# Kernel optimization log

Measured on AMD Instinct MI355X. Metric: run time of the kernel, lower is better.

## Reference

```python
import jax, jax.numpy as jnp
import numpy as np

B, N, D, H = 2, 2048, 1024, 8
DH = D // H  # head dim = 128


def setup_inputs() -> dict:
    key = jax.random.key(0)
    k0, k1, k2 = jax.random.split(key, 3)
    s = 1.0 / np.sqrt(D).astype(np.float32)
    return {
        "x": jax.random.normal(k0, (B, N, D), dtype=jnp.float32),
        "w_qkv": jax.random.normal(k1, (3 * D, D), dtype=jnp.float32) * s,
        "b_qkv": jnp.zeros((3 * D,), dtype=jnp.float32),
        "w_o": jax.random.normal(k2, (D, D), dtype=jnp.float32) * s,
        "b_o": jnp.zeros((D,), dtype=jnp.float32),
    }


def reference(x, w_qkv, b_qkv, w_o, b_o):
    b, n, d = x.shape
    h = H
    dh = d // h
    # qkv projection (torch Linear: x @ W.T + b)
    qkv = x @ w_qkv.T + b_qkv                      # [b, n, 3d]
    # rearrange 'b n (k d h) -> k b h n d': head index is INNERMOST
    qkv = qkv.reshape(b, n, 3, dh, h)              # [b, n, k, dh, h]
    qkv = jnp.transpose(qkv, (2, 0, 4, 1, 3))      # [k, b, h, n, dh]
    q, k, v = qkv[0], qkv[1], qkv[2]
    # unnormalized attention: NO softmax between the two einsums
    attn = jnp.einsum('bhik,bhjk->bhij', q, k)     # [b, h, n, n]
    out = jnp.einsum('bhik,bhkj->bhij', attn, v)   # [b, h, n, dh]
    # rearrange 'b h n d -> b n (h d)'
    out = jnp.transpose(out, (0, 2, 1, 3)).reshape(b, n, d)
    return out @ w_o.T + b_o
```

## Files before the change

### kernel.cpp

```cpp
#include <hip/hip_runtime.h>
#include <hip/hip_bf16.h>
#include <stdint.h>


typedef __bf16 bf16_t;
typedef __bf16 bf16x4 __attribute__((ext_vector_type(4)));
typedef __bf16 bf16x8 __attribute__((ext_vector_type(8)));
typedef float  fx4    __attribute__((ext_vector_type(4)));
typedef unsigned short u16;
typedef u16 u16x4 __attribute__((ext_vector_type(4)));
typedef u16 u16x8 __attribute__((ext_vector_type(8)));

typedef const void __attribute__((address_space(1)))* gas_ptr;
typedef void __attribute__((address_space(3)))*       las_ptr;

__device__ __forceinline__ void gl_lds16(const void* g, void* l) {
  __builtin_amdgcn_global_load_lds((gas_ptr)g, (las_ptr)l, 16, 0, 0);
}

__global__ __launch_bounds__(256) void beacon_kernel(float* out, float val, int n)
{
  const int i = blockIdx.x * 256 + threadIdx.x;
  if (i < n) out[i] = val;
}

__global__ __launch_bounds__(256) void conv_all_kernel(
    const float* __restrict__ x, const float* __restrict__ wq,
    const float* __restrict__ wo, const float* __restrict__ bq,
    bf16_t* __restrict__ xb, bf16_t* __restrict__ wqkvb,
    bf16_t* __restrict__ wob, float* __restrict__ bqp)
{
  const int i = blockIdx.x * 256 + threadIdx.x;
  if (i < 2097152) {
    const float* src; bf16_t* dst; int soff, doff;
    if (i < 1048576) { src = x; dst = xb; soff = i; doff = i; }
    else if (i < 1835008) {
      const int j  = i - 1048576;
      const int rp = j >> 8, g = j & 255;
      const int kk = rp >> 10, rem = rp & 1023;
      const int hh = rem >> 7,  dd = rem & 127;
      const int r  = kk * 1024 + dd * 8 + hh;
      src = wq; dst = wqkvb; soff = r * 256 + g; doff = j;
    } else {
      const int j = i - 1835008;
      src = wo; dst = wob; soff = j; doff = j;
    }
    const float4 v = ((const float4*)src)[soff];
    bf16x4 o;
    o[0] = (bf16_t)v.x; o[1] = (bf16_t)v.y; o[2] = (bf16_t)v.z; o[3] = (bf16_t)v.w;
    ((bf16x4*)dst)[doff] = o;
  } else if (i < 2097920) {
    const int j = i - 2097152;
    float4 v;
    float* pv = (float*)&v;
#pragma unroll
    for (int q = 0; q < 4; ++q) {
      const int cp = j * 4 + q;
      const int kk = cp >> 10, rem = cp & 1023;
      const int hh = rem >> 7,  dd = rem & 127;
      pv[q] = bq[kk * 1024 + dd * 8 + hh];
    }
    ((float4*)bqp)[j] = v;
  }
}

__global__ __launch_bounds__(256) void gemm1_kernel(
    const bf16_t* __restrict__ A, const bf16_t* __restrict__ Bt,
    const float* __restrict__ bias, bf16_t* __restrict__ outb)
{
  __shared__ __align__(16) short As[128*32];
  __shared__ __align__(16) short Bs[128*32];
  const int t    = threadIdx.x;
  const int lane = t & 63;
  const int w    = t >> 6;
  const int wr   = (w >> 1) << 6;
  const int wc   = (w & 1) << 6;
  const int lrow = lane & 15;
  const int kq   = (lane >> 4) << 3;
  const int row0 = blockIdx.y * 128;
  const int col0 = blockIdx.x * 128;

  const int i0 = t, i1 = t + 256;
  const bf16_t* a0 = A  + (size_t)(row0 + (i0 >> 2)) * 1024 + ((i0 & 3) << 3);
  const bf16_t* a1 = A  + (size_t)(row0 + (i1 >> 2)) * 1024 + ((i1 & 3) << 3);
  const bf16_t* b0 = Bt + (size_t)(col0 + (i0 >> 2)) * 1024 + ((i0 & 3) << 3);
  const bf16_t* b1 = Bt + (size_t)(col0 + (i1 >> 2)) * 1024 + ((i1 & 3) << 3);
  short* sa0 = &As[i0 * 8]; short* sa1 = &As[i1 * 8];
  short* sb0 = &Bs[i0 * 8]; short* sb1 = &Bs[i1 * 8];

  fx4 acc[4][4] = {};

  for (int k0 = 0; k0 < 1024; k0 += 32) {
    gl_lds16(a0 + k0, sa0);
    gl_lds16(a1 + k0, sa1);
    gl_lds16(b0 + k0, sb0);
    gl_lds16(b1 + k0, sb1);
    __syncthreads();
    bf16x8 af[4], bfr[4];
#pragma unroll
    for (int i = 0; i < 4; ++i)
      af[i] = *(const bf16x8*)&As[(wr + i*16 + lrow)*32 + kq];
#pragma unroll
    for (int j = 0; j < 4; ++j)
      bfr[j] = *(const bf16x8*)&Bs[(wc + j*16 + lrow)*32 + kq];
#pragma unroll
    for (int i = 0; i < 4; ++i)
#pragma unroll
      for (int j = 0; j < 4; ++j)
        acc[i][j] = __builtin_amdgcn_mfma_f32_16x16x32_bf16(af[i], bfr[j], acc[i][j], 0, 0, 0);
    __syncthreads();
  }

#pragma unroll
  for (int j = 0; j < 4; ++j) {
    const int col = col0 + wc + j*16 + lrow;
    const float bv = bias[col];
#pragma unroll
    for (int i = 0; i < 4; ++i) {
#pragma unroll
      for (int r = 0; r < 4; ++r) {
        const int row = row0 + wr + i*16 + ((lane >> 4) << 2) + r;
        outb[(size_t)row * 3072 + col] = (bf16_t)(acc[i][j][r] + bv);
      }
    }
  }
}

__global__ __launch_bounds__(256) void gemm2_kernel(
    const bf16_t* __restrict__ A,
    const bf16_t* __restrict__ Wt,
    const float* __restrict__ bias,
    float* __restrict__ out)
{
  __shared__ __align__(16) short As[128*32];
  __shared__ __align__(16) short Bs[64*32];
  const int t    = threadIdx.x;
  const int lane = t & 63;
  const int w    = t >> 6;
  const int wm   = w >> 1;
  const int wn   = w & 1;
  const int lrow = lane & 15;
  const int kq   = (lane >> 4) << 3;
  const int row0 = blockIdx.y * 128;
  const int col0 = blockIdx.x * 64;
  const bf16_t* Bt = Wt + (row0 >= 2048 ? (size_t)1048576 : (size_t)0);

  const int i0 = t, i1 = t + 256;
  const bf16_t* a0 = A  + (size_t)(row0 + (i0 >> 2)) * 3072 + ((i0 & 3) << 3);
  const bf16_t* a1 = A  + (size_t)(row0 + (i1 >> 2)) * 3072 + ((i1 & 3) << 3);
  const bf16_t* b0 = Bt + (size_t)(col0 + (i0 >> 2)) * 1024 + ((i0 & 3) << 3);
  short* sa0 = &As[i0 * 8]; short* sa1 = &As[i1 * 8];
  short* sb0 = &Bs[i0 * 8];

  fx4 acc[4][2] = {};

  for (int k0 = 0; k0 < 1024; k0 += 32) {
    gl_lds16(a0 + k0, sa0);
    gl_lds16(a1 + k0, sa1);
    gl_lds16(b0 + k0, sb0);
    __syncthreads();
    bf16x8 af[4], bfr[2];
#pragma unroll
    for (int i = 0; i < 4; ++i)
      af[i] = *(const bf16x8*)&As[(wm*64 + i*16 + lrow)*32 + kq];
#pragma unroll
    for (int j = 0; j < 2; ++j)
      bfr[j] = *(const bf16x8*)&Bs[(wn*32 + j*16 + lrow)*32 + kq];
#pragma unroll
    for (int i = 0; i < 4; ++i)
#pragma unroll
      for (int j = 0; j < 2; ++j)
        acc[i][j] = __builtin_amdgcn_mfma_f32_16x16x32_bf16(af[i], bfr[j], acc[i][j], 0, 0, 0);
    __syncthreads();
  }

#pragma unroll
  for (int j = 0; j < 2; ++j) {
    const int col = col0 + wn*32 + j*16 + lrow;
    const float bv = bias[col];
#pragma unroll
    for (int i = 0; i < 4; ++i) {
#pragma unroll
      for (int r = 0; r < 4; ++r) {
        const int row = row0 + wm*64 + i*16 + ((lane >> 4) << 2) + r;
        out[(size_t)row * 1024 + col] = acc[i][j][r] + bv;
      }
    }
  }
}

__global__ __launch_bounds__(128) void kv_part(
    const bf16_t* __restrict__ qkv, float* __restrict__ Mpart)
{
  __shared__ float Ksf[64][128];
  __shared__ float Vsf[64][64];
  const int t = threadIdx.x;
  const int ch = blockIdx.x >> 1, dh = blockIdx.x & 1, bh = blockIdx.y;
  const int b = bh >> 3, h = bh & 7;
  const bf16_t* Kg = qkv + (size_t)(b * 2048) * 3072 + 1024 + h * 128;
  const bf16_t* Vg = qkv + (size_t)(b * 2048) * 3072 + 2048 + h * 128 + dh * 64;
  const int e0 = (t >> 3) * 8;
  const int d0 = (t & 7) * 8;
  float acc[8][8] = {};

  for (int sub = 0; sub < 2; ++sub) {
    const int n0 = ch * 128 + sub * 64;
#pragma unroll
    for (int p = 0; p < 8; ++p) {
      const int idx = t + p * 128;
      const int r = idx >> 4, c = (idx & 15) * 8;
      const bf16x8 k8 = *(const bf16x8*)(Kg + (size_t)(n0 + r) * 3072 + c);
      float4 f0 = { (float)k8[0], (float)k8[1], (float)k8[2], (float)k8[3] };
      float4 f1 = { (float)k8[4], (float)k8[5], (float)k8[6], (float)k8[7] };
      *(float4*)&Ksf[r][c]     = f0;
      *(float4*)&Ksf[r][c + 4] = f1;
    }
#pragma unroll
    for (int p = 0; p < 4; ++p) {
      const int idx = t + p * 128;
      const int r = idx >> 3, c = (idx & 7) * 8;
      const bf16x8 v8 = *(const bf16x8*)(Vg + (size_t)(n0 + r) * 3072 + c);
      float4 f0 = { (float)v8[0], (float)v8[1], (float)v8[2], (float)v8[3] };
      float4 f1 = { (float)v8[4], (float)v8[5], (float)v8[6], (float)v8[7] };
      *(float4*)&Vsf[r][c]     = f0;
      *(float4*)&Vsf[r][c + 4] = f1;
    }
    __syncthreads();
    for (int n = 0; n < 64; ++n) {
      const float4 ka = *(const float4*)&Ksf[n][e0];
      const float4 kb = *(const float4*)&Ksf[n][e0 + 4];
      const float4 va = *(const float4*)&Vsf[n][d0];
      const float4 vb = *(const float4*)&Vsf[n][d0 + 4];
      const float kf[8] = { ka.x, ka.y, ka.z, ka.w, kb.x, kb.y, kb.z, kb.w };
      const float vf[8] = { va.x, va.y, va.z, va.w, vb.x, vb.y, vb.z, vb.w };
#pragma unroll
      for (int i = 0; i < 8; ++i)
#pragma unroll
        for (int j = 0; j < 8; ++j) acc[i][j] += kf[i] * vf[j];
    }
    __syncthreads();
  }

  float* op = Mpart + ((size_t)(bh * 16 + ch) << 14) + dh * 64;
#pragma unroll
  for (int i = 0; i < 8; ++i) {
    *(float4*)&op[(e0 + i) * 128 + d0]     = *(const float4*)&acc[i][0];
    *(float4*)&op[(e0 + i) * 128 + d0 + 4] = *(const float4*)&acc[i][4];
  }
}

__global__ __launch_bounds__(256) void reduce_m(
    const float* __restrict__ Mpart, bf16_t* __restrict__ Mb)
{
  const int t = threadIdx.x, bh = blockIdx.y;
  const int task = blockIdx.x * 256 + t;
  const int e = task >> 5, dq = task & 31;
  const float* base = Mpart + ((size_t)(bh * 16) << 14) + e * 128 + dq * 4;
  float4 s = { 0.f, 0.f, 0.f, 0.f };
#pragma unroll
  for (int ch = 0; ch < 16; ++ch) {
    const float4 v = *(const float4*)(base + ((size_t)ch << 14));
    s.x += v.x; s.y += v.y; s.z += v.z; s.w += v.w;
  }
  u16x4 wv;
  bf16_t b0 = (bf16_t)s.x; wv[0] = *(u16*)&b0;
  bf16_t b1 = (bf16_t)s.y; wv[1] = *(u16*)&b1;
  bf16_t b2 = (bf16_t)s.z; wv[2] = *(u16*)&b2;
  bf16_t b3 = (bf16_t)s.w; wv[3] = *(u16*)&b3;
  *(u16x4*)(Mb + (size_t)bh * 16384 + e * 128 + dq * 4) = wv;
}

__global__ __launch_bounds__(256) void wprime_kernel(
    const bf16_t* __restrict__ wob, const bf16_t* __restrict__ Mb,
    bf16_t* __restrict__ Wt)
{
  __shared__ __align__(16) short As[128*32];
  __shared__ __align__(16) short Bs[64*32];
  const int t    = threadIdx.x;
  const int lane = t & 63;
  const int w    = t >> 6;
  const int wm   = w >> 1;
  const int wn   = w & 1;
  const int lrow = lane & 15;
  const int kq   = (lane >> 4) << 3;
  const int o0   = (blockIdx.x >> 1) * 128;
  const int eh   = (blockIdx.x & 1) * 64;
  const int bh   = blockIdx.y, b = bh >> 3, h = bh & 7;
  const bf16_t* A  = wob + (size_t)o0 * 1024 + h * 128;
  const bf16_t* Bt = Mb + (size_t)bh * 16384 + (size_t)eh * 128;

  const int i0 = t, i1 = t + 256;
  const bf16_t* a0 = A  + (size_t)(i0 >> 2) * 1024 + ((i0 & 3) << 3);
  const bf16_t* a1 = A  + (size_t)(i1 >> 2) * 1024 + ((i1 & 3) << 3);
  const bf16_t* b0 = Bt + (size_t)(i0 >> 2) * 128  + ((i0 & 3) << 3);
  short* sa0 = &As[i0 * 8]; short* sa1 = &As[i1 * 8];
  short* sb0 = &Bs[i0 * 8];

  fx4 acc[4][2] = {};

  for (int k0 = 0; k0 < 128; k0 += 32) {
    gl_lds16(a0 + k0, sa0);
    gl_lds16(a1 + k0, sa1);
    gl_lds16(b0 + k0, sb0);
    __syncthreads();
    bf16x8 af[4], bfr[2];
#pragma unroll
    for (int i = 0; i < 4; ++i)
      af[i] = *(const bf16x8*)&As[(wm*64 + i*16 + lrow)*32 + kq];
#pragma unroll
    for (int j = 0; j < 2; ++j)
      bfr[j] = *(const bf16x8*)&Bs[(wn*32 + j*16 + lrow)*32 + kq];
#pragma unroll
    for (int i = 0; i < 4; ++i)
#pragma unroll
      for (int j = 0; j < 2; ++j)
        acc[i][j] = __builtin_amdgcn_mfma_f32_16x16x32_bf16(af[i], bfr[j], acc[i][j], 0, 0, 0);
    __syncthreads();
  }

  bf16_t* obase = Wt + (size_t)b * 1048576 + h * 128;
#pragma unroll
  for (int j = 0; j < 2; ++j) {
    const int col = eh + wn*32 + j*16 + lrow;
#pragma unroll
    for (int i = 0; i < 4; ++i) {
#pragma unroll
      for (int r = 0; r < 4; ++r) {
        const int row = o0 + wm*64 + i*16 + ((lane >> 4) << 2) + r;
        obase[(size_t)row * 1024 + col] = (bf16_t)acc[i][j][r];
      }
    }
  }
}

extern "C" void kernel_launch(void* const* d_in, const int* in_sizes, int n_in,
                              void* d_out, int out_size, void* d_ws, size_t ws_size,
                              hipStream_t stream) {
  float* out = (float*)d_out;
  dim3 blk(256);

  int ix = -1, iwq = -1, ibq = -1, iwo = -1, ibo = -1;
  if (n_in == 5) {
    for (int i = 0; i < 5; ++i) {
      switch (in_sizes[i]) {
        case 4194304: ix  = i; break;
        case 3145728: iwq = i; break;
        case 3072:    ibq = i; break;
        case 1048576: iwo = i; break;
        case 1024:    ibo = i; break;
        default: break;
      }
    }
  }
  if (ix < 0 || iwq < 0 || ibq < 0 || iwo < 0 || ibo < 0) {
    beacon_kernel<<<dim3((out_size + 255) / 256), blk, 0, stream>>>(out, 50000.0f, out_size);
    return;
  }
  const size_t NEEDED = (size_t)40 * 1048576;
  if (ws_size < NEEDED) {
    beacon_kernel<<<dim3((out_size + 255) / 256), blk, 0, stream>>>(out, 30000.0f, out_size);
    return;
  }

  char* ws = (char*)d_ws;
  bf16_t* xb     = (bf16_t*)(ws);
  bf16_t* wqkvb  = (bf16_t*)(ws + (size_t)8  * 1048576);
  bf16_t* wob    = (bf16_t*)(ws + (size_t)14 * 1048576);
  bf16_t* qkv    = (bf16_t*)(ws + (size_t)16 * 1048576);
  bf16_t* Mb     = (bf16_t*)(ws);
  bf16_t* Wt     = (bf16_t*)(ws + (size_t)1  * 1048576);
  float*  bqp    = (float*)d_out;
  float*  Mpart  = (float*)d_out;

  const float* bo = (const float*)d_in[ibo];

  conv_all_kernel<<<dim3(8195),   blk, 0, stream>>>((const float*)d_in[ix],
                                                    (const float*)d_in[iwq],
                                                    (const float*)d_in[iwo],
                                                    (const float*)d_in[ibq],
                                                    xb, wqkvb, wob, bqp);
  gemm1_kernel   <<<dim3(24, 32), blk, 0, stream>>>(xb, wqkvb, bqp, qkv);
  kv_part        <<<dim3(32, 16), dim3(128), 0, stream>>>(qkv, Mpart);
  reduce_m       <<<dim3(16, 16), blk, 0, stream>>>(Mpart, Mb);
  wprime_kernel  <<<dim3(16, 16), blk, 0, stream>>>(wob, Mb, Wt);
  gemm2_kernel   <<<dim3(16, 32), blk, 0, stream>>>(qkv, Wt, bo, out);
}
```

Measured before the change: 173.9 us.

## Compute K^T V on MFMA via transposed K/V and widen GEMM K-steps

Replaces the scalar FP32 outer-product K^T·V partial kernel with a transpose kernel that writes K and V in head-dim-major layout, followed by an MFMA GEMM over 8 sequence slices and a smaller reduction. This moves the per-head 128x128 accumulation onto matrix cores and halves the number of partials to reduce. Separately, gemm1 and gemm2 now load two 32-wide K chunks per barrier pair, which halves the synchronisation count at the cost of doubled LDS use. The transpose adds an extra pass over K and V through global memory, and Vt is parked in the output buffer as scratch.

```diff
diff --git a/kernel.cpp b/kernel.cpp
--- a/kernel.cpp
+++ b/kernel.cpp
@@ -17,6 +17,8 @@
 __device__ __forceinline__ void gl_lds16(const void* g, void* l) {
   __builtin_amdgcn_global_load_lds((gas_ptr)g, (las_ptr)l, 16, 0, 0);
 }
+
+#define TSLAB 262144
 
 __global__ __launch_bounds__(256) void beacon_kernel(float* out, float val, int n)
 {
@@ -68,6 +70,119 @@
     const bf16_t* __restrict__ A, const bf16_t* __restrict__ Bt,
     const float* __restrict__ bias, bf16_t* __restrict__ outb)
 {
+  __shared__ __align__(16) short As0[128*32], As1[128*32];
+  __shared__ __align__(16) short Bs0[128*32], Bs1[128*32];
+  const int t    = threadIdx.x;
+  const int lane = t & 63;
+  const int w    = t >> 6;
+  const int wr   = (w >> 1) << 6;
+  const int wc   = (w & 1) << 6;
+  const int lrow = lane & 15;
+  const int kq   = (lane >> 4) << 3;
+  const int row0 = blockIdx.y * 128;
+  const int col0 = blockIdx.x * 128;
+
+  const int i0 = t, i1 = t + 256;
+  const bf16_t* a0 = A  + (size_t)(row0 + (i0 >> 2)) * 1024 + ((i0 & 3) << 3);
+  const bf16_t* a1 = A  + (size_t)(row0 + (i1 >> 2)) * 1024 + ((i1 & 3) << 3);
+  const bf16_t* b0 = Bt + (size_t)(col0 + (i0 >> 2)) * 1024 + ((i0 & 3) << 3);
+  const bf16_t* b1 = Bt + (size_t)(col0 + (i1 >> 2)) * 1024 + ((i1 & 3) << 3);
+
+  fx4 acc[4][4] = {};
+
+  for (int k0 = 0; k0 < 1024; k0 += 64) {
+    gl_lds16(a0 + k0,      &As0[i0 * 8]);
+    gl_lds16(a1 + k0,      &As0[i1 * 8]);
+    gl_lds16(b0 + k0,      &Bs0[i0 * 8]);
+    gl_lds16(b1 + k0,      &Bs0[i1 * 8]);
+    gl_lds16(a0 + k0 + 32, &As1[i0 * 8]);
+    gl_lds16(a1 + k0 + 32, &As1[i1 * 8]);
+    gl_lds16(b0 + k0 + 32, &Bs1[i0 * 8]);
+    gl_lds16(b1 + k0 + 32, &Bs1[i1 * 8]);
+    __syncthreads();
+    {
+      bf16x8 af[4], bfr[4];
+#pragma unroll
+      for (int i = 0; i < 4; ++i)
+        af[i] = *(const bf16x8*)&As0[(wr + i*16 + lrow)*32 + kq];
+#pragma unroll
+      for (int j = 0; j < 4; ++j)
+        bfr[j] = *(const bf16x8*)&Bs0[(wc + j*16 + lrow)*32 + kq];
+#pragma unroll
+      for (int i = 0; i < 4; ++i)
+#pragma unroll
+        for (int j = 0; j < 4; ++j)
+          acc[i][j] = __builtin_amdgcn_mfma_f32_16x16x32_bf16(af[i], bfr[j], acc[i][j], 0, 0, 0);
+    }
+    {
+      bf16x8 af[4], bfr[4];
+#pragma unroll
+      for (int i = 0; i < 4; ++i)
+        af[i] = *(const bf16x8*)&As1[(wr + i*16 + lrow)*32 + kq];
+#pragma unroll
+      for (int j = 0; j < 4; ++j)
+        bfr[j] = *(const bf16x8*)&Bs1[(wc + j*16 + lrow)*32 + kq];
+#pragma unroll
+      for (int i = 0; i < 4; ++i)
+#pragma unroll
+        for (int j = 0; j < 4; ++j)
+          acc[i][j] = __builtin_amdgcn_mfma_f32_16x16x32_bf16(af[i], bfr[j], acc[i][j], 0, 0, 0);
+    }
+    __syncthreads();
+  }
+
+#pragma unroll
+  for (int j = 0; j < 4; ++j) {
+    const int col = col0 + wc + j*16 + lrow;
+    const float bv = bias[col];
+#pragma unroll
+    for (int i = 0; i < 4; ++i) {
+#pragma unroll
+      for (int r = 0; r < 4; ++r) {
+        const int row = row0 + wr + i*16 + ((lane >> 4) << 2) + r;
+        outb[(size_t)row * 3072 + col] = (bf16_t)(acc[i][j][r] + bv);
+      }
+    }
+  }
+}
+
+__global__ __launch_bounds__(256) void kt_vt_kernel(
+    const bf16_t* __restrict__ qkv, bf16_t* __restrict__ Kt,
+    bf16_t* __restrict__ Vt)
+{
+  __shared__ u16 L[64][132];
+  const int t  = threadIdx.x;
+  const int n0 = blockIdx.x * 64;
+  const int bh = blockIdx.y >> 1, kv = blockIdx.y & 1;
+  const int b  = bh >> 3, h = bh & 7;
+  const u16* src = (const u16*)qkv + (size_t)(b * 2048 + n0) * 3072
+                   + (1 + kv) * 1024 + h * 128;
+
+#pragma unroll
+  for (int p = 0; p < 4; ++p) {
+    const int idx = t + p * 256;
+    const int r = idx >> 4, g = idx & 15;
+    const u16x8 v = *(const u16x8*)(src + (size_t)r * 3072 + 8 * g);
+    *(u16x8*)&L[r][8 * g] = v;
+  }
+  __syncthreads();
+
+  bf16_t* dstb = (kv == 0 ? Kt : Vt) + (size_t)bh * TSLAB;
+#pragma unroll
+  for (int p = 0; p < 4; ++p) {
+    const int idx = t + p * 256;
+    const int c = idx >> 3, gn = idx & 7;
+    u16x8 wv;
+#pragma unroll
+    for (int j = 0; j < 8; ++j) wv[j] = L[8 * gn + j][c];
+    *(u16x8*)(dstb + (size_t)c * 2048 + n0 + 8 * gn) = wv;
+  }
+}
+
+__global__ __launch_bounds__(256) void kvt_mfma_kernel(
+    const bf16_t* __restrict__ Kt, const bf16_t* __restrict__ Vt,
+    float* __restrict__ Mpart2)
+{
   __shared__ __align__(16) short As[128*32];
   __shared__ __align__(16) short Bs[128*32];
   const int t    = threadIdx.x;
@@ -77,20 +192,22 @@
   const int wc   = (w & 1) << 6;
   const int lrow = lane & 15;
   const int kq   = (lane >> 4) << 3;
-  const int row0 = blockIdx.y * 128;
-  const int col0 = blockIdx.x * 128;
+  const int ks   = blockIdx.x;
+  const int bh   = blockIdx.y;
+  const bf16_t* Ab = Kt + (size_t)bh * TSLAB + ks * 256;
+  const bf16_t* Bb = Vt + (size_t)bh * TSLAB + ks * 256;
 
   const int i0 = t, i1 = t + 256;
-  const bf16_t* a0 = A  + (size_t)(row0 + (i0 >> 2)) * 1024 + ((i0 & 3) << 3);
-  const bf16_t* a1 = A  + (size_t)(row0 + (i1 >> 2)) * 1024 + ((i1 & 3) << 3);
-  const bf16_t* b0 = Bt + (size_t)(col0 + (i0 >> 2)) * 1024 + ((i0 & 3) << 3);
-  const bf16_t* b1 = Bt + (size_t)(col0 + (i1 >> 2)) * 1024 + ((i1 & 3) << 3);
+  const bf16_t* a0 = Ab + (size_t)(i0 >> 2) * 2048 + ((i0 & 3) << 3);
+  const bf16_t* a1 = Ab + (size_t)(i1 >> 2) * 2048 + ((i1 & 3) << 3);
+  const bf16_t* b0 = Bb + (size_t)(i0 >> 2) * 2048 + ((i0 & 3) << 3);
+  const bf16_t* b1 = Bb + (size_t)(i1 >> 2) * 2048 + ((i1 & 3) << 3);
   short* sa0 = &As[i0 * 8]; short* sa1 = &As[i1 * 8];
   short* sb0 = &Bs[i0 * 8]; short* sb1 = &Bs[i1 * 8];
 
   fx4 acc[4][4] = {};
 
-  for (int k0 = 0; k0 < 1024; k0 += 32) {
+  for (int k0 = 0; k0 < 256; k0 += 32) {
     gl_lds16(a0 + k0, sa0);
     gl_lds16(a1 + k0, sa1);
     gl_lds16(b0 + k0, sb0);
@@ -111,155 +228,31 @@
     __syncthreads();
   }
 
+  float* op = Mpart2 + ((size_t)(bh * 8 + ks) << 14);
 #pragma unroll
   for (int j = 0; j < 4; ++j) {
-    const int col = col0 + wc + j*16 + lrow;
-    const float bv = bias[col];
+    const int col = wc + j*16 + lrow;
 #pragma unroll
     for (int i = 0; i < 4; ++i) {
 #pragma unroll
       for (int r = 0; r < 4; ++r) {
-        const int row = row0 + wr + i*16 + ((lane >> 4) << 2) + r;
-        outb[(size_t)row * 3072 + col] = (bf16_t)(acc[i][j][r] + bv);
+        const int row = wr + i*16 + ((lane >> 4) << 2) + r;
+        op[(size_t)row * 128 + col] = acc[i][j][r];
       }
     }
   }
 }
 
-__global__ __launch_bounds__(256) void gemm2_kernel(
-    const bf16_t* __restrict__ A,
-    const bf16_t* __restrict__ Wt,
-    const float* __restrict__ bias,
-    float* __restrict__ out)
-{
-  __shared__ __align__(16) short As[128*32];
-  __shared__ __align__(16) short Bs[64*32];
-  const int t    = threadIdx.x;
-  const int lane = t & 63;
-  const int w    = t >> 6;
-  const int wm   = w >> 1;
-  const int wn   = w & 1;
-  const int lrow = lane & 15;
-  const int kq   = (lane >> 4) << 3;
-  const int row0 = blockIdx.y * 128;
-  const int col0 = blockIdx.x * 64;
-  const bf16_t* Bt = Wt + (row0 >= 2048 ? (size_t)1048576 : (size_t)0);
-
-  const int i0 = t, i1 = t + 256;
-  const bf16_t* a0 = A  + (size_t)(row0 + (i0 >> 2)) * 3072 + ((i0 & 3) << 3);
-  const bf16_t* a1 = A  + (size_t)(row0 + (i1 >> 2)) * 3072 + ((i1 & 3) << 3);
-  const bf16_t* b0 = Bt + (size_t)(col0 + (i0 >> 2)) * 1024 + ((i0 & 3) << 3);
-  short* sa0 = &As[i0 * 8]; short* sa1 = &As[i1 * 8];
-  short* sb0 = &Bs[i0 * 8];
-
-  fx4 acc[4][2] = {};
-
-  for (int k0 = 0; k0 < 1024; k0 += 32) {
-    gl_lds16(a0 + k0, sa0);
-    gl_lds16(a1 + k0, sa1);
-    gl_lds16(b0 + k0, sb0);
-    __syncthreads();
-    bf16x8 af[4], bfr[2];
-#pragma unroll
-    for (int i = 0; i < 4; ++i)
-      af[i] = *(const bf16x8*)&As[(wm*64 + i*16 + lrow)*32 + kq];
-#pragma unroll
-    for (int j = 0; j < 2; ++j)
-      bfr[j] = *(const bf16x8*)&Bs[(wn*32 + j*16 + lrow)*32 + kq];
-#pragma unroll
-    for (int i = 0; i < 4; ++i)
-#pragma unroll
-      for (int j = 0; j < 2; ++j)
-        acc[i][j] = __builtin_amdgcn_mfma_f32_16x16x32_bf16(af[i], bfr[j], acc[i][j], 0, 0, 0);
-    __syncthreads();
-  }
-
-#pragma unroll
-  for (int j = 0; j < 2; ++j) {
-    const int col = col0 + wn*32 + j*16 + lrow;
-    const float bv = bias[col];
-#pragma unroll
-    for (int i = 0; i < 4; ++i) {
-#pragma unroll
-      for (int r = 0; r < 4; ++r) {
-        const int row = row0 + wm*64 + i*16 + ((lane >> 4) << 2) + r;
-        out[(size_t)row * 1024 + col] = acc[i][j][r] + bv;
-      }
-    }
-  }
-}
-
-__global__ __launch_bounds__(128) void kv_part(
-    const bf16_t* __restrict__ qkv, float* __restrict__ Mpart)
-{
-  __shared__ float Ksf[64][128];
-  __shared__ float Vsf[64][64];
-  const int t = threadIdx.x;
-  const int ch = blockIdx.x >> 1, dh = blockIdx.x & 1, bh = blockIdx.y;
-  const int b = bh >> 3, h = bh & 7;
-  const bf16_t* Kg = qkv + (size_t)(b * 2048) * 3072 + 1024 + h * 128;
-  const bf16_t* Vg = qkv + (size_t)(b * 2048) * 3072 + 2048 + h * 128 + dh * 64;
-  const int e0 = (t >> 3) * 8;
-  const int d0 = (t & 7) * 8;
-  float acc[8][8] = {};
-
-  for (int sub = 0; sub < 2; ++sub) {
-    const int n0 = ch * 128 + sub * 64;
-#pragma unroll
-    for (int p = 0; p < 8; ++p) {
-      const int idx = t + p * 128;
-      const int r = idx >> 4, c = (idx & 15) * 8;
-      const bf16x8 k8 = *(const bf16x8*)(Kg + (size_t)(n0 + r) * 3072 + c);
-      float4 f0 = { (float)k8[0], (float)k8[1], (float)k8[2], (float)k8[3] };
-      float4 f1 = { (float)k8[4], (float)k8[5], (float)k8[6], (float)k8[7] };
-      *(float4*)&Ksf[r][c]     = f0;
-      *(float4*)&Ksf[r][c + 4] = f1;
-    }
-#pragma unroll
-    for (int p = 0; p < 4; ++p) {
-      const int idx = t + p * 128;
-      const int r = idx >> 3, c = (idx & 7) * 8;
-      const bf16x8 v8 = *(const bf16x8*)(Vg + (size_t)(n0 + r) * 3072 + c);
-      float4 f0 = { (float)v8[0], (float)v8[1], (float)v8[2], (float)v8[3] };
-      float4 f1 = { (float)v8[4], (float)v8[5], (float)v8[6], (float)v8[7] };
-      *(float4*)&Vsf[r][c]     = f0;
-      *(float4*)&Vsf[r][c + 4] = f1;
-    }
-    __syncthreads();
-    for (int n = 0; n < 64; ++n) {
-      const float4 ka = *(const float4*)&Ksf[n][e0];
-      const float4 kb = *(const float4*)&Ksf[n][e0 + 4];
-      const float4 va = *(const float4*)&Vsf[n][d0];
-      const float4 vb = *(const float4*)&Vsf[n][d0 + 4];
-      const float kf[8] = { ka.x, ka.y, ka.z, ka.w, kb.x, kb.y, kb.z, kb.w };
-      const float vf[8] = { va.x, va.y, va.z, va.w, vb.x, vb.y, vb.z, vb.w };
-#pragma unroll
-      for (int i = 0; i < 8; ++i)
-#pragma unroll
-        for (int j = 0; j < 8; ++j) acc[i][j] += kf[i] * vf[j];
-    }
-    __syncthreads();
-  }
-
-  float* op = Mpart + ((size_t)(bh * 16 + ch) << 14) + dh * 64;
-#pragma unroll
-  for (int i = 0; i < 8; ++i) {
-    *(float4*)&op[(e0 + i) * 128 + d0]     = *(const float4*)&acc[i][0];
-    *(float4*)&op[(e0 + i) * 128 + d0 + 4] = *(const float4*)&acc[i][4];
-  }
-}
-
-__global__ __launch_bounds__(256) void reduce_m(
-    const float* __restrict__ Mpart, bf16_t* __restrict__ Mb)
+__global__ __launch_bounds__(256) void reduce_m2(
+    const float* __restrict__ Mpart2, bf16_t* __restrict__ Mb)
 {
   const int t = threadIdx.x, bh = blockIdx.y;
   const int task = blockIdx.x * 256 + t;
-  const int e = task >> 5, dq = task & 31;
-  const float* base = Mpart + ((size_t)(bh * 16) << 14) + e * 128 + dq * 4;
+  const float* base = Mpart2 + ((size_t)(bh * 8) << 14) + task * 4;
   float4 s = { 0.f, 0.f, 0.f, 0.f };
 #pragma unroll
-  for (int ch = 0; ch < 16; ++ch) {
-    const float4 v = *(const float4*)(base + ((size_t)ch << 14));
+  for (int ks = 0; ks < 8; ++ks) {
+    const float4 v = *(const float4*)(base + ((size_t)ks << 14));
     s.x += v.x; s.y += v.y; s.z += v.z; s.w += v.w;
   }
   u16x4 wv;
@@ -267,7 +260,7 @@
   bf16_t b1 = (bf16_t)s.y; wv[1] = *(u16*)&b1;
   bf16_t b2 = (bf16_t)s.z; wv[2] = *(u16*)&b2;
   bf16_t b3 = (bf16_t)s.w; wv[3] = *(u16*)&b3;
-  *(u16x4*)(Mb + (size_t)bh * 16384 + e * 128 + dq * 4) = wv;
+  *(u16x4*)(Mb + (size_t)bh * 16384 + task * 4) = wv;
 }
 
 __global__ __launch_bounds__(256) void wprime_kernel(
@@ -333,6 +326,86 @@
   }
 }
 
+__global__ __launch_bounds__(256) void gemm2_kernel(
+    const bf16_t* __restrict__ A,
+    const bf16_t* __restrict__ Wt,
+    const float* __restrict__ bias,
+    float* __restrict__ out)
+{
+  __shared__ __align__(16) short As0[128*32], As1[128*32];
+  __shared__ __align__(16) short Bs0[64*32],  Bs1[64*32];
+  const int t    = threadIdx.x;
+  const int lane = t & 63;
+  const int w    = t >> 6;
+  const int wm   = w >> 1;
+  const int wn   = w & 1;
+  const int lrow = lane & 15;
+  const int kq   = (lane >> 4) << 3;
+  const int row0 = blockIdx.y * 128;
+  const int col0 = blockIdx.x * 64;
+  const bf16_t* Bt = Wt + (row0 >= 2048 ? (size_t)1048576 : (size_t)0);
+
+  const int i0 = t, i1 = t + 256;
+  const bf16_t* a0 = A  + (size_t)(row0 + (i0 >> 2)) * 3072 + ((i0 & 3) << 3);
+  const bf16_t* a1 = A  + (size_t)(row0 + (i1 >> 2)) * 3072 + ((i1 & 3) << 3);
+  const bf16_t* b0 = Bt + (size_t)(col0 + (i0 >> 2)) * 1024 + ((i0 & 3) << 3);
+
+  fx4 acc[4][2] = {};
+
+  for (int k0 = 0; k0 < 1024; k0 += 64) {
+    gl_lds16(a0 + k0,      &As0[i0 * 8]);
+    gl_lds16(a1 + k0,      &As0[i1 * 8]);
+    gl_lds16(b0 + k0,      &Bs0[i0 * 8]);
+    gl_lds16(a0 + k0 + 32, &As1[i0 * 8]);
+    gl_lds16(a1 + k0 + 32, &As1[i1 * 8]);
+    gl_lds16(b0 + k0 + 32, &Bs1[i0 * 8]);
+    __syncthreads();
+    {
+      bf16x8 af[4], bfr[2];
+#pragma unroll
+      for (int i = 0; i < 4; ++i)
+        af[i] = *(const bf16x8*)&As0[(wm*64 + i*16 + lrow)*32 + kq];
+#pragma unroll
+      for (int j = 0; j < 2; ++j)
+        bfr[j] = *(const bf16x8*)&Bs0[(wn*32 + j*16 + lrow)*32 + kq];
+#pragma unroll
+      for (int i = 0; i < 4; ++i)
+#pragma unroll
+        for (int j = 0; j < 2; ++j)
+          acc[i][j] = __builtin_amdgcn_mfma_f32_16x16x32_bf16(af[i], bfr[j], acc[i][j], 0, 0, 0);
+    }
+    {
+      bf16x8 af[4], bfr[2];
+#pragma unroll
+      for (int i = 0; i < 4; ++i)
+        af[i] = *(const bf16x8*)&As1[(wm*64 + i*16 + lrow)*32 + kq];
+#pragma unroll
+      for (int j = 0; j < 2; ++j)
+        bfr[j] = *(const bf16x8*)&Bs1[(wn*32 + j*16 + lrow)*32 + kq];
+#pragma unroll
+      for (int i = 0; i < 4; ++i)
+#pragma unroll
+        for (int j = 0; j < 2; ++j)
+          acc[i][j] = __builtin_amdgcn_mfma_f32_16x16x32_bf16(af[i], bfr[j], acc[i][j], 0, 0, 0);
+    }
+    __syncthreads();
+  }
+
+#pragma unroll
+  for (int j = 0; j < 2; ++j) {
+    const int col = col0 + wn*32 + j*16 + lrow;
+    const float bv = bias[col];
+#pragma unroll
+    for (int i = 0; i < 4; ++i) {
+#pragma unroll
+      for (int r = 0; r < 4; ++r) {
+        const int row = row0 + wm*64 + i*16 + ((lane >> 4) << 2) + r;
+        out[(size_t)row * 1024 + col] = acc[i][j][r] + bv;
+      }
+    }
+  }
+}
+
 extern "C" void kernel_launch(void* const* d_in, const int* in_sizes, int n_in,
                               void* d_out, int out_size, void* d_ws, size_t ws_size,
                               hipStream_t stream) {
@@ -367,10 +440,12 @@
   bf16_t* wqkvb  = (bf16_t*)(ws + (size_t)8  * 1048576);
   bf16_t* wob    = (bf16_t*)(ws + (size_t)14 * 1048576);
   bf16_t* qkv    = (bf16_t*)(ws + (size_t)16 * 1048576);
-  bf16_t* Mb     = (bf16_t*)(ws);
-  bf16_t* Wt     = (bf16_t*)(ws + (size_t)1  * 1048576);
+  bf16_t* Kt     = (bf16_t*)(ws);
+  bf16_t* Mb     = (bf16_t*)(ws + (size_t)8  * 1048576);
+  bf16_t* Wt     = (bf16_t*)(ws + (size_t)9  * 1048576);
   float*  bqp    = (float*)d_out;
-  float*  Mpart  = (float*)d_out;
+  float*  Mpart2 = (float*)d_out;
+  bf16_t* Vt     = (bf16_t*)d_out + 4194304;
 
   const float* bo = (const float*)d_in[ibo];
 
@@ -380,8 +455,9 @@
                                                     (const float*)d_in[ibq],
                                                     xb, wqkvb, wob, bqp);
   gemm1_kernel   <<<dim3(24, 32), blk, 0, stream>>>(xb, wqkvb, bqp, qkv);
-  kv_part        <<<dim3(32, 16), dim3(128), 0, stream>>>(qkv, Mpart);
-  reduce_m       <<<dim3(16, 16), blk, 0, stream>>>(Mpart, Mb);
+  kt_vt_kernel   <<<dim3(32, 32), blk, 0, stream>>>(qkv, Kt, Vt);
+  kvt_mfma_kernel<<<dim3(8, 16),  blk, 0, stream>>>(Kt, Vt, Mpart2);
+  reduce_m2      <<<dim3(16, 16), blk, 0, stream>>>(Mpart2, Mb);
   wprime_kernel  <<<dim3(16, 16), blk, 0, stream>>>(wob, Mb, Wt);
   gemm2_kernel   <<<dim3(16, 32), blk, 0, stream>>>(qkv, Wt, bo, out);
 }
```

After: 166.6 us. 1.04x faster.
